# Kernel optimization log

Measured on AMD Instinct MI355X. Metric: run time of the kernel, lower is better.

Reference implementation:

```python
import jax, jax.numpy as jnp
import numpy as np

N, E, FDIM, HID, HEADS, C, L, G = 50000, 800000, 512, 256, 8, 32, 3, 64
EPS = 1e-5


def setup_inputs() -> dict:
    key = jax.random.key(0)
    ks = jax.random.split(key, 16)
    x = jax.random.normal(ks[0], (N, FDIM), dtype=jnp.float32)
    edge_index = jax.random.randint(ks[1], (2, E), 0, N, dtype=jnp.int32)
    batch = jnp.sort(jax.random.randint(ks[2], (N,), 0, G, dtype=jnp.int32))
    s = lambda f: 1.0 / np.sqrt(f)
    return {
        "x": x,
        "edge_index": edge_index,
        "batch": batch,
        "in_w": jax.random.normal(ks[3], (FDIM, HID), jnp.float32) * s(FDIM),
        "in_b": jnp.zeros((HID,), jnp.float32),
        "gat_w": jax.random.normal(ks[4], (L, HID, HID), jnp.float32) * s(HID),
        "att_src": jax.random.normal(ks[5], (L, HEADS, C), jnp.float32) * s(C),
        "att_dst": jax.random.normal(ks[6], (L, HEADS, C), jnp.float32) * s(C),
        "gat_b": jnp.zeros((L, HID), jnp.float32),
        "res_w": jax.random.normal(ks[7], (L, HID, HID), jnp.float32) * s(HID),
        "res_b": jnp.zeros((L, HID), jnp.float32),
        "ln_g": jnp.ones((L, HID), jnp.float32),
        "ln_b": jnp.zeros((L, HID), jnp.float32),
        "pool_w": jax.random.normal(ks[8], (2 * HID, HID), jnp.float32) * s(2 * HID),
        "pool_b": jnp.zeros((HID,), jnp.float32),
    }


def _gat_layer(h, src, dst, w, a_src, a_dst, b):
    # PyG GATConv, concat=True, negative_slope=0.2, dropout inactive (eval)
    xh = (h @ w).reshape(N, HEADS, C)                      # [N,H,C]
    asn = jnp.einsum('nhc,hc->nh', xh, a_src)              # [N,H]
    adn = jnp.einsum('nhc,hc->nh', xh, a_dst)
    e = jax.nn.leaky_relu(asn[src] + adn[dst], 0.2)        # [E2,H]
    # scatter-softmax over destination neighborhoods
    m = jax.ops.segment_max(e, dst, num_segments=N)
    m = jnp.where(jnp.isfinite(m), m, 0.0)
    ex = jnp.exp(e - m[dst])
    den = jax.ops.segment_sum(ex, dst, num_segments=N)
    alpha = ex / (den[dst] + 1e-16)                        # [E2,H]
    msg = xh[src] * alpha[:, :, None]                      # [E2,H,C]
    out = jax.ops.segment_sum(msg, dst, num_segments=N)    # [N,H,C]
    return out.reshape(N, HID) + b


def _layer_norm(h, g, b):
    mu = jnp.mean(h, axis=-1, keepdims=True)
    var = jnp.mean((h - mu) ** 2, axis=-1, keepdims=True)
    return (h - mu) * jax.lax.rsqrt(var + EPS) * g + b


def reference(x, edge_index, batch, in_w, in_b, gat_w, att_src, att_dst, gat_b,
              res_w, res_b, ln_g, ln_b, pool_w, pool_b):
    loops = jnp.arange(N, dtype=edge_index.dtype)          # GATConv add_self_loops=True
    src = jnp.concatenate([edge_index[0], loops])
    dst = jnp.concatenate([edge_index[1], loops])
    h = x @ in_w + in_b
    for i in range(L):
        h_res = h @ res_w[i] + res_b[i]
        h = _gat_layer(h, src, dst, gat_w[i], att_src[i], att_dst[i], gat_b[i])
        h = jax.nn.relu(_layer_norm(h + h_res, ln_g[i], ln_b[i]))
    ones = jnp.ones((N,), h.dtype)
    cnt = jax.ops.segment_sum(ones, batch, num_segments=G)
    h_mean = jax.ops.segment_sum(h, batch, num_segments=G) / jnp.maximum(cnt, 1.0)[:, None]
    h_max = jax.ops.segment_max(h, batch, num_segments=G)
    h_cat = jnp.concatenate([h_mean, h_max], axis=1)       # [G, 2*HID]
    return jax.nn.relu(h_cat @ pool_w + pool_b)            # [G, HID]
```

## Files before the change

### kernel.cpp

```cpp
#include <hip/hip_runtime.h>
#include <math.h>

#define N_NODES 50000
#define E_EDGES 800000
#define E2 (E_EDGES + N_NODES)
#define M_PAD 50048
#define FDIM 512
#define HID 256
#define HEADS 8
#define CDIM 32
#define LAYERS 3
#define GRAPHS 64
#define LN_EPS 1e-5f
#define POOL_P 16

typedef unsigned short ushort_t;
typedef __attribute__((ext_vector_type(8))) short short8v;
typedef __attribute__((ext_vector_type(4))) float f32x4;

__device__ __forceinline__ float bf2f(ushort_t u) {
    union { unsigned int i; float f; } v;
    v.i = ((unsigned int)u) << 16;
    return v.f;
}
__device__ __forceinline__ ushort_t f2bf(float f) {
    union { float f; unsigned int u; } v;
    v.f = f;
    unsigned int r = (v.u + 0x7FFFu + ((v.u >> 16) & 1u)) >> 16;
    return (ushort_t)r;
}
__device__ __forceinline__ void gload_lds16(const void* g, void* l) {
    __builtin_amdgcn_global_load_lds(
        (const __attribute__((address_space(1))) void*)g,
        (__attribute__((address_space(3))) void*)l, 16, 0, 0);
}

__global__ void k_count(const int* __restrict__ ei, int* __restrict__ cnt) {
    int e = blockIdx.x * 256 + threadIdx.x;
    if (e >= E2) return;
    int dst = (e < E_EDGES) ? ei[E_EDGES + e] : (e - E_EDGES);
    atomicAdd(&cnt[dst], 1);
}

__global__ void k_scan1(const int* __restrict__ cnt, int* __restrict__ part) {
    __shared__ int s[256];
    int t = threadIdx.x;
    int i = blockIdx.x * 256 + t;
    s[t] = (i < N_NODES) ? cnt[i] : 0;
    __syncthreads();
    for (int d = 128; d > 0; d >>= 1) {
        if (t < d) s[t] += s[t + d];
        __syncthreads();
    }
    if (t == 0) part[blockIdx.x] = s[0];
}

__global__ void k_scan2(int* __restrict__ part, int nb, int* __restrict__ rowptr) {
    __shared__ int s[256];
    int t = threadIdx.x;
    int v = (t < nb) ? part[t] : 0;
    s[t] = v;
    __syncthreads();
    for (int d = 1; d < 256; d <<= 1) {
        int x = (t >= d) ? s[t - d] : 0;
        __syncthreads();
        s[t] += x;
        __syncthreads();
    }
    if (t < nb) part[t] = s[t] - v;
    if (t == 255) rowptr[N_NODES] = s[255];
}

__global__ void k_scan3(const int* __restrict__ cnt, const int* __restrict__ part,
                        int* __restrict__ rowptr) {
    __shared__ int s[256];
    int t = threadIdx.x;
    int i = blockIdx.x * 256 + t;
    int v = (i < N_NODES) ? cnt[i] : 0;
    s[t] = v;
    __syncthreads();
    for (int d = 1; d < 256; d <<= 1) {
        int x = (t >= d) ? s[t - d] : 0;
        __syncthreads();
        s[t] += x;
        __syncthreads();
    }
    if (i < N_NODES) rowptr[i] = part[blockIdx.x] + s[t] - v;
}

__global__ void k_fill(const int* __restrict__ ei, const int* __restrict__ rowptr,
                       int* __restrict__ fill, int* __restrict__ colv) {
    int e = blockIdx.x * 256 + threadIdx.x;
    if (e >= E2) return;
    int src, dst;
    if (e < E_EDGES) { src = ei[e]; dst = ei[E_EDGES + e]; }
    else             { src = dst = e - E_EDGES; }
    int pos = atomicAdd(&fill[dst], 1);
    colv[rowptr[dst] + pos] = src;
}

__global__ void k_bounds(const int* __restrict__ batch, int* __restrict__ rowstart) {
    int n = blockIdx.x * 256 + threadIdx.x;
    if (n >= N_NODES) return;
    int b = batch[n];
    int bp = (n == 0) ? -1 : batch[n - 1];
    for (int g = bp + 1; g <= b; ++g) rowstart[g] = n;
    if (n == N_NODES - 1) {
        for (int g = b + 1; g <= GRAPHS; ++g) rowstart[g] = N_NODES;
    }
}

__global__ __launch_bounds__(256) void k_cast_x(const float* __restrict__ x,
                                                ushort_t* __restrict__ xb) {
    long long i8 = ((long long)blockIdx.x * 256 + threadIdx.x) * 8;
    if (i8 >= (long long)M_PAD * FDIM) return;
    int row = (int)(i8 >> 9);
    ushort_t o[8];
    if (row < N_NODES) {
        const float* p = x + i8;
        #pragma unroll
        for (int j = 0; j < 8; ++j) o[j] = f2bf(p[j]);
    } else {
        #pragma unroll
        for (int j = 0; j < 8; ++j) o[j] = 0;
    }
    *(short8v*)(xb + i8) = *(short8v*)o;
}

__global__ __launch_bounds__(256) void k_wtrans(const float* __restrict__ W,
                                                ushort_t* __restrict__ WT, int K) {
    int i = blockIdx.x * 256 + threadIdx.x;
    if (i >= K * HID) return;
    int k = i >> 8, n = i & 255;
    WT[(size_t)n * K + k] = f2bf(W[i]);
}

template<int K>
__global__ __launch_bounds__(256) void k_gemm_bf16(const ushort_t* __restrict__ A,
                                                   const ushort_t* __restrict__ BT,
                                                   const float* __restrict__ bias0,
                                                   const float* __restrict__ bias1,
                                                   ushort_t* __restrict__ C0,
                                                   ushort_t* __restrict__ C1, int M) {
    __shared__ char lds[16384] __attribute__((aligned(16)));
    const int bm = blockIdx.x * 128;
    const int bn = blockIdx.y * 128;
    const int t = threadIdx.x, w = t >> 6, l = t & 63;
    const int wr = w >> 1, wc = w & 1;

    const int c1 = t, c2 = t + 256;
    const int ar1 = c1 >> 2, as1 = (c1 & 3) ^ ((ar1 >> 1) & 3);
    const int ar2 = c2 >> 2, as2 = (c2 & 3) ^ ((ar2 >> 1) & 3);
    const ushort_t* pa1 = A + (size_t)(bm + ar1) * K + as1 * 8;
    const ushort_t* pa2 = A + (size_t)(bm + ar2) * K + as2 * 8;
    const ushort_t* pb1 = BT + (size_t)(bn + ar1) * K + as1 * 8;
    const ushort_t* pb2 = BT + (size_t)(bn + ar2) * K + as2 * 8;
    char* la1 = lds + w * 1024;
    char* la2 = lds + 4096 + w * 1024;
    char* lb1 = lds + 8192 + w * 1024;
    char* lb2 = lds + 12288 + w * 1024;

    int aoff[4], boff[4];
    const int kb = l >> 4;
    #pragma unroll
    for (int mi = 0; mi < 4; ++mi) {
        int r = wr * 64 + mi * 16 + (l & 15);
        aoff[mi] = r * 64 + ((kb ^ ((r >> 1) & 3)) << 4);
        int c = wc * 64 + mi * 16 + (l & 15);
        boff[mi] = 8192 + c * 64 + ((kb ^ ((c >> 1) & 3)) << 4);
    }

    f32x4 acc[4][4] = {};
    for (int k0 = 0; k0 < K; k0 += 32) {
        gload_lds16(pa1 + k0, la1);
        gload_lds16(pa2 + k0, la2);
        gload_lds16(pb1 + k0, lb1);
        gload_lds16(pb2 + k0, lb2);
        __syncthreads();
        short8v a[4], b[4];
        #pragma unroll
        for (int mi = 0; mi < 4; ++mi) a[mi] = *(const short8v*)(lds + aoff[mi]);
        #pragma unroll
        for (int ni = 0; ni < 4; ++ni) b[ni] = *(const short8v*)(lds + boff[ni]);
        #pragma unroll
        for (int mi = 0; mi < 4; ++mi)
            #pragma unroll
            for (int ni = 0; ni < 4; ++ni)
                acc[mi][ni] = __builtin_amdgcn_mfma_f32_16x16x32_bf16(
                    a[mi], b[ni], acc[mi][ni], 0, 0, 0);
        __syncthreads();
    }

    ushort_t* C = (bn < 256) ? C0 : C1;
    const float* bias = (bn < 256) ? bias0 : bias1;
    const int cb = (bn < 256) ? bn : bn - 256;
    #pragma unroll
    for (int mi = 0; mi < 4; ++mi) {
        int row = bm + wr * 64 + mi * 16 + (l >> 4) * 4;
        #pragma unroll
        for (int ni = 0; ni < 4; ++ni) {
            int col = cb + wc * 64 + ni * 16 + (l & 15);
            float bv = bias ? bias[col] : 0.f;
            #pragma unroll
            for (int r = 0; r < 4; ++r) {
                if (row + r < M)
                    C[(size_t)(row + r) * HID + col] = f2bf(acc[mi][ni][r] + bv);
            }
        }
    }
}

__global__ __launch_bounds__(256) void k_scores(const ushort_t* __restrict__ xhb,
                                                const float* __restrict__ a_src,
                                                const float* __restrict__ a_dst,
                                                float* __restrict__ asn,
                                                float* __restrict__ adn) {
    int wave = threadIdx.x >> 6, lane = threadIdx.x & 63;
    int n = blockIdx.x * 4 + wave;
    if (n >= N_NODES) return;
    int head = lane >> 3, part = lane & 7;
    ushort4 u = *(const ushort4*)(xhb + (size_t)n * HID + head * CDIM + part * 4);
    float vx = bf2f(u.x), vy = bf2f(u.y), vz = bf2f(u.z), vw = bf2f(u.w);
    const float4 ws = *(const float4*)(a_src + head * CDIM + part * 4);
    const float4 wd = *(const float4*)(a_dst + head * CDIM + part * 4);
    float ds_ = vx * ws.x + vy * ws.y + vz * ws.z + vw * ws.w;
    float dd_ = vx * wd.x + vy * wd.y + vz * wd.z + vw * wd.w;
    for (int d = 1; d < 8; d <<= 1) {
        ds_ += __shfl_xor(ds_, d);
        dd_ += __shfl_xor(dd_, d);
    }
    if (part == 0) {
        asn[n * HEADS + head] = ds_;
        adn[n * HEADS + head] = dd_;
    }
}

__global__ __launch_bounds__(256) void k_agg_ln(const ushort_t* __restrict__ xhb,
                                                const float* __restrict__ asn,
                                                const float* __restrict__ adn,
                                                const int* __restrict__ rowptr,
                                                const int* __restrict__ colv,
                                                const ushort_t* __restrict__ hresb,
                                                const float* __restrict__ gb,
                                                const float* __restrict__ g,
                                                const float* __restrict__ b,
                                                ushort_t* __restrict__ hb) {
    int wave = threadIdx.x >> 6, lane = threadIdx.x & 63;
    int n = blockIdx.x * 4 + wave;
    if (n >= N_NODES) return;
    int head = lane >> 3, part = lane & 7;
    int c0 = head * CDIM + part * 4;
    float adn_h = adn[n * HEADS + head];
    int j0 = rowptr[n], j1 = rowptr[n + 1];
    float den = 0.f;
    float a0 = 0.f, a1 = 0.f, a2 = 0.f, a3 = 0.f;
    int j = j0;
    for (; j + 3 < j1; j += 4) {
        int s0 = colv[j], s1 = colv[j + 1], s2 = colv[j + 2], s3 = colv[j + 3];
        ushort4 u0 = *(const ushort4*)(xhb + (size_t)s0 * HID + c0);
        ushort4 u1 = *(const ushort4*)(xhb + (size_t)s1 * HID + c0);
        ushort4 u2 = *(const ushort4*)(xhb + (size_t)s2 * HID + c0);
        ushort4 u3 = *(const ushort4*)(xhb + (size_t)s3 * HID + c0);
        float e0 = asn[s0 * HEADS + head] + adn_h;
        float e1 = asn[s1 * HEADS + head] + adn_h;
        float e2 = asn[s2 * HEADS + head] + adn_h;
        float e3 = asn[s3 * HEADS + head] + adn_h;
        e0 = (e0 > 0.f) ? e0 : 0.2f * e0;
        e1 = (e1 > 0.f) ? e1 : 0.2f * e1;
        e2 = (e2 > 0.f) ? e2 : 0.2f * e2;
        e3 = (e3 > 0.f) ? e3 : 0.2f * e3;
        float p0 = __expf(e0), p1 = __expf(e1), p2 = __expf(e2), p3 = __expf(e3);
        den += (p0 + p1) + (p2 + p3);
        a0 += p0 * bf2f(u0.x) + p1 * bf2f(u1.x) + p2 * bf2f(u2.x) + p3 * bf2f(u3.x);
        a1 += p0 * bf2f(u0.y) + p1 * bf2f(u1.y) + p2 * bf2f(u2.y) + p3 * bf2f(u3.y);
        a2 += p0 * bf2f(u0.z) + p1 * bf2f(u1.z) + p2 * bf2f(u2.z) + p3 * bf2f(u3.z);
        a3 += p0 * bf2f(u0.w) + p1 * bf2f(u1.w) + p2 * bf2f(u2.w) + p3 * bf2f(u3.w);
    }
    for (; j < j1; ++j) {
        int s = colv[j];
        ushort4 u = *(const ushort4*)(xhb + (size_t)s * HID + c0);
        float e = asn[s * HEADS + head] + adn_h;
        e = (e > 0.f) ? e : 0.2f * e;
        float p = __expf(e);
        den += p;
        a0 += p * bf2f(u.x);
        a1 += p * bf2f(u.y);
        a2 += p * bf2f(u.z);
        a3 += p * bf2f(u.w);
    }
    float inv = 1.f / (den + 1e-16f);
    ushort4 hr = *(const ushort4*)(hresb + (size_t)n * HID + c0);
    float4 gb4 = *(const float4*)(gb + c0);
    float v0 = a0 * inv + bf2f(hr.x) + gb4.x;
    float v1 = a1 * inv + bf2f(hr.y) + gb4.y;
    float v2 = a2 * inv + bf2f(hr.z) + gb4.z;
    float v3 = a3 * inv + bf2f(hr.w) + gb4.w;
    float s = v0 + v1 + v2 + v3;
    for (int d = 1; d < 64; d <<= 1) s += __shfl_xor(s, d);
    float mu = s * (1.f / HID);
    float d0 = v0 - mu, d1 = v1 - mu, d2 = v2 - mu, d3 = v3 - mu;
    float q = d0 * d0 + d1 * d1 + d2 * d2 + d3 * d3;
    for (int d = 1; d < 64; d <<= 1) q += __shfl_xor(q, d);
    float rstd = rsqrtf(q * (1.f / HID) + LN_EPS);
    float4 gg = *(const float4*)(g + c0);
    float4 bb = *(const float4*)(b + c0);
    ushort_t o[4];
    o[0] = f2bf(fmaxf(d0 * rstd * gg.x + bb.x, 0.f));
    o[1] = f2bf(fmaxf(d1 * rstd * gg.y + bb.y, 0.f));
    o[2] = f2bf(fmaxf(d2 * rstd * gg.z + bb.z, 0.f));
    o[3] = f2bf(fmaxf(d3 * rstd * gg.w + bb.w, 0.f));
    *(ushort4*)(hb + (size_t)n * HID + c0) = *(ushort4*)o;
}

__global__ __launch_bounds__(256) void k_pool1(const ushort_t* __restrict__ hb,
                                               const int* __restrict__ rowstart,
                                               float* __restrict__ part) {
    int g = blockIdx.x, p = blockIdx.y, c = threadIdx.x;
    int s0 = rowstart[g], s1 = rowstart[g + 1];
    float sum = 0.f, mx = -INFINITY;
    for (int n = s0 + p; n < s1; n += POOL_P) {
        float v = bf2f(hb[(size_t)n * HID + c]);
        sum += v;
        mx = fmaxf(mx, v);
    }
    float* pp = part + (size_t)(g * POOL_P + p) * 512;
    pp[c] = sum;
    pp[256 + c] = mx;
}

__global__ __launch_bounds__(256) void k_pool2(const float* __restrict__ part,
                                               const int* __restrict__ rowstart,
                                               float* __restrict__ hcat) {
    int g = blockIdx.x, c = threadIdx.x;
    float sum = 0.f, mx = -INFINITY;
    for (int p = 0; p < POOL_P; ++p) {
        const float* pp = part + (size_t)(g * POOL_P + p) * 512;
        sum += pp[c];
        mx = fmaxf(mx, pp[256 + c]);
    }
    float cntf = (float)(rowstart[g + 1] - rowstart[g]);
    hcat[(size_t)g * (2 * HID) + c] = sum / fmaxf(cntf, 1.f);
    hcat[(size_t)g * (2 * HID) + HID + c] = mx;
}

__global__ __launch_bounds__(256) void k_pool_gemm(const float* __restrict__ hcat,
                                                   const float* __restrict__ W,
                                                   const float* __restrict__ bias,
                                                   float* __restrict__ out) {
    int g = blockIdx.x, c = threadIdx.x;
    const float* hg = hcat + (size_t)g * (2 * HID);
    float acc = bias[c];
    for (int k = 0; k < 2 * HID; ++k)
        acc += hg[k] * W[(size_t)k * HID + c];
    out[(size_t)g * HID + c] = fmaxf(acc, 0.f);
}

extern "C" void kernel_launch(void* const* d_in, const int* in_sizes, int n_in,
                              void* d_out, int out_size, void* d_ws, size_t ws_size,
                              hipStream_t stream) {
    const float* x       = (const float*)d_in[0];
    const int*   ei      = (const int*)d_in[1];
    const int*   batch   = (const int*)d_in[2];
    const float* in_w    = (const float*)d_in[3];
    const float* in_b    = (const float*)d_in[4];
    const float* gat_w   = (const float*)d_in[5];
    const float* att_src = (const float*)d_in[6];
    const float* att_dst = (const float*)d_in[7];
    const float* gat_b   = (const float*)d_in[8];
    const float* res_w   = (const float*)d_in[9];
    const float* res_b   = (const float*)d_in[10];
    const float* ln_g    = (const float*)d_in[11];
    const float* ln_b    = (const float*)d_in[12];
    const float* pool_w  = (const float*)d_in[13];
    const float* pool_b  = (const float*)d_in[14];
    float* out = (float*)d_out;

    char* ws = (char*)d_ws;
    size_t off = 0;
    auto alloc = [&](size_t bytes) -> char* {
        char* p = ws + off;
        off = (off + bytes + 255) & ~(size_t)255;
        return p;
    };
    ushort_t* xb    = (ushort_t*)alloc((size_t)M_PAD * FDIM * 2);
    ushort_t* hb    = (ushort_t*)alloc((size_t)M_PAD * HID * 2);
    ushort_t* xhb   = (ushort_t*)alloc((size_t)M_PAD * HID * 2);
    ushort_t* hresb = (ushort_t*)alloc((size_t)M_PAD * HID * 2);
    float* asn      = (float*)alloc((size_t)N_NODES * HEADS * 4);
    float* adn      = (float*)alloc((size_t)N_NODES * HEADS * 4);
    int*   cnt      = (int*)alloc((size_t)N_NODES * 4);
    int*   fill     = (int*)alloc((size_t)N_NODES * 4);
    int*   rowptr   = (int*)alloc((size_t)(N_NODES + 1) * 4);
    int*   colv     = (int*)alloc((size_t)E2 * 4);
    int*   part     = (int*)alloc(256 * 4);
    int*   rowstart = (int*)alloc((size_t)(GRAPHS + 1) * 4);
    ushort_t* wt_in = (ushort_t*)alloc((size_t)HID * FDIM * 2);
    ushort_t* wt2   = (ushort_t*)alloc((size_t)LAYERS * 512 * HID * 2);
    float* poolpart = (float*)alloc((size_t)GRAPHS * POOL_P * 512 * 4);
    float* hcat     = (float*)alloc((size_t)GRAPHS * 2 * HID * 4);

    hipMemsetAsync(cnt, 0, (size_t)N_NODES * 4, stream);
    hipMemsetAsync(fill, 0, (size_t)N_NODES * 4, stream);

    const int ge = (E2 + 255) / 256;
    const int nb = (N_NODES + 255) / 256;
    k_count<<<ge, 256, 0, stream>>>(ei, cnt);
    k_scan1<<<nb, 256, 0, stream>>>(cnt, part);
    k_scan2<<<1, 256, 0, stream>>>(part, nb, rowptr);
    k_scan3<<<nb, 256, 0, stream>>>(cnt, part, rowptr);
    k_fill<<<ge, 256, 0, stream>>>(ei, rowptr, fill, colv);
    k_bounds<<<nb, 256, 0, stream>>>(batch, rowstart);

    k_cast_x<<<(int)(((size_t)M_PAD * FDIM / 8 + 255) / 256), 256, 0, stream>>>(x, xb);
    k_wtrans<<<(FDIM * HID + 255) / 256, 256, 0, stream>>>(in_w, wt_in, FDIM);
    for (int i = 0; i < LAYERS; ++i) {
        ushort_t* w2 = wt2 + (size_t)i * 512 * HID;
        k_wtrans<<<(HID * HID + 255) / 256, 256, 0, stream>>>(
            res_w + (size_t)i * HID * HID, w2, HID);
        k_wtrans<<<(HID * HID + 255) / 256, 256, 0, stream>>>(
            gat_w + (size_t)i * HID * HID, w2 + (size_t)256 * HID, HID);
    }

    dim3 gg1(M_PAD / 128, 2);
    k_gemm_bf16<FDIM><<<gg1, 256, 0, stream>>>(xb, wt_in, in_b, nullptr,
                                               hb, nullptr, N_NODES);

    const int nw = (N_NODES + 3) / 4;
    dim3 gg2(M_PAD / 128, 4);
    for (int i = 0; i < LAYERS; ++i) {
        k_gemm_bf16<HID><<<gg2, 256, 0, stream>>>(hb, wt2 + (size_t)i * 512 * HID,
                                                  res_b + (size_t)i * HID, nullptr,
                                                  hresb, xhb, N_NODES);
        k_scores<<<nw, 256, 0, stream>>>(xhb, att_src + (size_t)i * HEADS * CDIM,
                                         att_dst + (size_t)i * HEADS * CDIM, asn, adn);
        k_agg_ln<<<nw, 256, 0, stream>>>(xhb, asn, adn, rowptr, colv, hresb,
                                         gat_b + (size_t)i * HID,
                                         ln_g + (size_t)i * HID,
                                         ln_b + (size_t)i * HID, hb);
    }
    dim3 pg(GRAPHS, POOL_P);
    k_pool1<<<pg, 256, 0, stream>>>(hb, rowstart, poolpart);
    k_pool2<<<GRAPHS, 256, 0, stream>>>(poolpart, rowstart, hcat);
    k_pool_gemm<<<GRAPHS, 256, 0, stream>>>(hcat, pool_w, pool_b, out);
}
```

Before: 609.7 us.

## Widen aggregation gathers to 16-byte loads with two edges per wave

The aggregation kernel now has each lane load 8 bf16 channels (16 bytes) instead of 4. The two half-waves each process a different neighbor edge, which doubles the number of edges in flight per wave, and the partial sums are combined with a cross-half shuffle before the fused LayerNorm. The seven weight-transpose launches are also merged into one kernel. The aim is higher memory-level parallelism in the gather-bound aggregation and less launch overhead. In exchange it adds a cross-lane reduction, a padded tail loop, and stores from only half the lanes.

```diff
diff --git a/kernel.cpp b/kernel.cpp
--- a/kernel.cpp
+++ b/kernel.cpp
@@ -127,12 +127,30 @@
     *(short8v*)(xb + i8) = *(short8v*)o;
 }
 
-__global__ __launch_bounds__(256) void k_wtrans(const float* __restrict__ W,
-                                                ushort_t* __restrict__ WT, int K) {
-    int i = blockIdx.x * 256 + threadIdx.x;
-    if (i >= K * HID) return;
-    int k = i >> 8, n = i & 255;
-    WT[(size_t)n * K + k] = f2bf(W[i]);
+#define IN_ELEMS (FDIM * HID)
+#define MAT_ELEMS (HID * HID)
+#define WT_TOTAL (IN_ELEMS + 2 * LAYERS * MAT_ELEMS)
+__global__ __launch_bounds__(256) void k_wtrans_all(const float* __restrict__ in_w,
+                                                    const float* __restrict__ gat_w,
+                                                    const float* __restrict__ res_w,
+                                                    ushort_t* __restrict__ wt_in,
+                                                    ushort_t* __restrict__ wt2) {
+    int id = blockIdx.x * 256 + threadIdx.x;
+    if (id >= WT_TOTAL) return;
+    if (id < IN_ELEMS) {
+        int k = id >> 8, n = id & 255;
+        wt_in[(size_t)n * FDIM + k] = f2bf(in_w[id]);
+    } else {
+        int r = id - IN_ELEMS;
+        int mat = r >> 16;
+        int layer = mat >> 1;
+        int isgat = mat & 1;
+        int within = r & 65535;
+        int k = within >> 8, n = within & 255;
+        const float* W = (isgat ? gat_w : res_w) + (size_t)layer * MAT_ELEMS;
+        wt2[(size_t)layer * 512 * HID + (size_t)(isgat * 256 + n) * HID + k] =
+            f2bf(W[within]);
+    }
 }
 
 template<int K>
@@ -245,71 +263,96 @@
                                                 const float* __restrict__ g,
                                                 const float* __restrict__ b,
                                                 ushort_t* __restrict__ hb) {
-    int wave = threadIdx.x >> 6, lane = threadIdx.x & 63;
-    int n = blockIdx.x * 4 + wave;
+    const int wave = threadIdx.x >> 6, lane = threadIdx.x & 63;
+    const int n = blockIdx.x * 4 + wave;
     if (n >= N_NODES) return;
-    int head = lane >> 3, part = lane & 7;
-    int c0 = head * CDIM + part * 4;
-    float adn_h = adn[n * HEADS + head];
-    int j0 = rowptr[n], j1 = rowptr[n + 1];
+    const int half = lane >> 5;
+    const int lh = lane & 31;
+    const int head = lh >> 2;
+    const int ch0 = lh * 8;
+    const float adn_h = adn[n * HEADS + head];
+    const int j0 = rowptr[n], j1 = rowptr[n + 1];
+
+    float acc[8] = {};
     float den = 0.f;
-    float a0 = 0.f, a1 = 0.f, a2 = 0.f, a3 = 0.f;
-    int j = j0;
-    for (; j + 3 < j1; j += 4) {
-        int s0 = colv[j], s1 = colv[j + 1], s2 = colv[j + 2], s3 = colv[j + 3];
-        ushort4 u0 = *(const ushort4*)(xhb + (size_t)s0 * HID + c0);
-        ushort4 u1 = *(const ushort4*)(xhb + (size_t)s1 * HID + c0);
-        ushort4 u2 = *(const ushort4*)(xhb + (size_t)s2 * HID + c0);
-        ushort4 u3 = *(const ushort4*)(xhb + (size_t)s3 * HID + c0);
-        float e0 = asn[s0 * HEADS + head] + adn_h;
-        float e1 = asn[s1 * HEADS + head] + adn_h;
-        float e2 = asn[s2 * HEADS + head] + adn_h;
-        float e3 = asn[s3 * HEADS + head] + adn_h;
-        e0 = (e0 > 0.f) ? e0 : 0.2f * e0;
-        e1 = (e1 > 0.f) ? e1 : 0.2f * e1;
-        e2 = (e2 > 0.f) ? e2 : 0.2f * e2;
-        e3 = (e3 > 0.f) ? e3 : 0.2f * e3;
-        float p0 = __expf(e0), p1 = __expf(e1), p2 = __expf(e2), p3 = __expf(e3);
-        den += (p0 + p1) + (p2 + p3);
-        a0 += p0 * bf2f(u0.x) + p1 * bf2f(u1.x) + p2 * bf2f(u2.x) + p3 * bf2f(u3.x);
-        a1 += p0 * bf2f(u0.y) + p1 * bf2f(u1.y) + p2 * bf2f(u2.y) + p3 * bf2f(u3.y);
-        a2 += p0 * bf2f(u0.z) + p1 * bf2f(u1.z) + p2 * bf2f(u2.z) + p3 * bf2f(u3.z);
-        a3 += p0 * bf2f(u0.w) + p1 * bf2f(u1.w) + p2 * bf2f(u2.w) + p3 * bf2f(u3.w);
-    }
-    for (; j < j1; ++j) {
-        int s = colv[j];
-        ushort4 u = *(const ushort4*)(xhb + (size_t)s * HID + c0);
+    int base = j0;
+    for (; base + 8 <= j1; base += 8) {
+        int idx[4];
+        #pragma unroll
+        for (int q = 0; q < 4; ++q) idx[q] = colv[base + 2 * q + half];
+        short8v u[4];
+        #pragma unroll
+        for (int q = 0; q < 4; ++q)
+            u[q] = *(const short8v*)(xhb + (size_t)idx[q] * HID + ch0);
+        float p[4];
+        #pragma unroll
+        for (int q = 0; q < 4; ++q) {
+            float e = asn[idx[q] * HEADS + head] + adn_h;
+            e = (e > 0.f) ? e : 0.2f * e;
+            p[q] = __expf(e);
+        }
+        #pragma unroll
+        for (int q = 0; q < 4; ++q) {
+            den += p[q];
+            #pragma unroll
+            for (int c = 0; c < 8; ++c)
+                acc[c] += p[q] * bf2f((ushort_t)u[q][c]);
+        }
+    }
+    for (; base < j1; base += 2) {
+        bool valid = (base + half) < j1;
+        int s = valid ? colv[base + half] : n;
+        short8v u = *(const short8v*)(xhb + (size_t)s * HID + ch0);
         float e = asn[s * HEADS + head] + adn_h;
         e = (e > 0.f) ? e : 0.2f * e;
-        float p = __expf(e);
+        float p = valid ? __expf(e) : 0.f;
         den += p;
-        a0 += p * bf2f(u.x);
-        a1 += p * bf2f(u.y);
-        a2 += p * bf2f(u.z);
-        a3 += p * bf2f(u.w);
-    }
-    float inv = 1.f / (den + 1e-16f);
-    ushort4 hr = *(const ushort4*)(hresb + (size_t)n * HID + c0);
-    float4 gb4 = *(const float4*)(gb + c0);
-    float v0 = a0 * inv + bf2f(hr.x) + gb4.x;
-    float v1 = a1 * inv + bf2f(hr.y) + gb4.y;
-    float v2 = a2 * inv + bf2f(hr.z) + gb4.z;
-    float v3 = a3 * inv + bf2f(hr.w) + gb4.w;
-    float s = v0 + v1 + v2 + v3;
-    for (int d = 1; d < 64; d <<= 1) s += __shfl_xor(s, d);
-    float mu = s * (1.f / HID);
-    float d0 = v0 - mu, d1 = v1 - mu, d2 = v2 - mu, d3 = v3 - mu;
-    float q = d0 * d0 + d1 * d1 + d2 * d2 + d3 * d3;
-    for (int d = 1; d < 64; d <<= 1) q += __shfl_xor(q, d);
-    float rstd = rsqrtf(q * (1.f / HID) + LN_EPS);
-    float4 gg = *(const float4*)(g + c0);
-    float4 bb = *(const float4*)(b + c0);
-    ushort_t o[4];
-    o[0] = f2bf(fmaxf(d0 * rstd * gg.x + bb.x, 0.f));
-    o[1] = f2bf(fmaxf(d1 * rstd * gg.y + bb.y, 0.f));
-    o[2] = f2bf(fmaxf(d2 * rstd * gg.z + bb.z, 0.f));
-    o[3] = f2bf(fmaxf(d3 * rstd * gg.w + bb.w, 0.f));
-    *(ushort4*)(hb + (size_t)n * HID + c0) = *(ushort4*)o;
+        #pragma unroll
+        for (int c = 0; c < 8; ++c)
+            acc[c] += p * bf2f((ushort_t)u[c]);
+    }
+    den += __shfl_xor(den, 32);
+    #pragma unroll
+    for (int c = 0; c < 8; ++c) acc[c] += __shfl_xor(acc[c], 32);
+
+    const float inv = 1.f / (den + 1e-16f);
+    short8v hr = *(const short8v*)(hresb + (size_t)n * HID + ch0);
+    float4 gbA = *(const float4*)(gb + ch0);
+    float4 gbB = *(const float4*)(gb + ch0 + 4);
+    float v[8];
+    #pragma unroll
+    for (int c = 0; c < 8; ++c) {
+        float gbv = (c < 4) ? ((const float*)&gbA)[c] : ((const float*)&gbB)[c - 4];
+        v[c] = acc[c] * inv + bf2f((ushort_t)hr[c]) + gbv;
+    }
+    float s = 0.f;
+    #pragma unroll
+    for (int c = 0; c < 8; ++c) s += v[c];
+    #pragma unroll
+    for (int d = 1; d < 32; d <<= 1) s += __shfl_xor(s, d);
+    const float mu = s * (1.f / HID);
+    float q = 0.f;
+    #pragma unroll
+    for (int c = 0; c < 8; ++c) {
+        v[c] -= mu;
+        q += v[c] * v[c];
+    }
+    #pragma unroll
+    for (int d = 1; d < 32; d <<= 1) q += __shfl_xor(q, d);
+    const float rstd = rsqrtf(q * (1.f / HID) + LN_EPS);
+    float4 gA = *(const float4*)(g + ch0);
+    float4 gB = *(const float4*)(g + ch0 + 4);
+    float4 bA = *(const float4*)(b + ch0);
+    float4 bB = *(const float4*)(b + ch0 + 4);
+    ushort_t o[8];
+    #pragma unroll
+    for (int c = 0; c < 8; ++c) {
+        float gv = (c < 4) ? ((const float*)&gA)[c] : ((const float*)&gB)[c - 4];
+        float bv = (c < 4) ? ((const float*)&bA)[c] : ((const float*)&bB)[c - 4];
+        o[c] = f2bf(fmaxf(v[c] * rstd * gv + bv, 0.f));
+    }
+    if (half == 0)
+        *(short8v*)(hb + (size_t)n * HID + ch0) = *(short8v*)o;
 }
 
 __global__ __launch_bounds__(256) void k_pool1(const ushort_t* __restrict__ hb,
@@ -412,14 +455,8 @@
     k_bounds<<<nb, 256, 0, stream>>>(batch, rowstart);
 
     k_cast_x<<<(int)(((size_t)M_PAD * FDIM / 8 + 255) / 256), 256, 0, stream>>>(x, xb);
-    k_wtrans<<<(FDIM * HID + 255) / 256, 256, 0, stream>>>(in_w, wt_in, FDIM);
-    for (int i = 0; i < LAYERS; ++i) {
-        ushort_t* w2 = wt2 + (size_t)i * 512 * HID;
-        k_wtrans<<<(HID * HID + 255) / 256, 256, 0, stream>>>(
-            res_w + (size_t)i * HID * HID, w2, HID);
-        k_wtrans<<<(HID * HID + 255) / 256, 256, 0, stream>>>(
-            gat_w + (size_t)i * HID * HID, w2 + (size_t)256 * HID, HID);
-    }
+    k_wtrans_all<<<(WT_TOTAL + 255) / 256, 256, 0, stream>>>(in_w, gat_w, res_w,
+                                                             wt_in, wt2);
 
     dim3 gg1(M_PAD / 128, 2);
     k_gemm_bf16<FDIM><<<gg1, 256, 0, stream>>>(xb, wt_in, in_b, nullptr,
```

New measurement: 587.5 us. -3.6%, faster.
